# Kernel optimization log

Measured on AMD Instinct MI355X. Metric: run time of the kernel, lower is better.

The kernel has to match this reference:

```python
import jax, jax.numpy as jnp
import numpy as np

N_NODES = 4096
NUM_REL = 200
D = 32
E = 16384
B = 2048
NEG = -1e30  # finite stand-in for -inf (nan-safe under vjp)


def setup_inputs() -> dict:
    key = jax.random.key(0)
    ks = jax.random.split(key, 8)
    return {
        "edge_src": jax.random.randint(ks[0], (E,), 0, N_NODES),
        "edge_dst": jax.random.randint(ks[1], (E,), 0, N_NODES),
        "edge_type": jax.random.randint(ks[2], (E,), 0, NUM_REL),
        "neighbor_edges": jnp.arange(B),  # distinct edge ids (torch.unique output)
        "neighbor_edges2rels": jax.random.randint(ks[3], (B,), 0, NUM_REL),
        "rel_emb": jax.random.normal(ks[4], (NUM_REL, D), dtype=jnp.float32),
        "W1": jax.random.normal(ks[5], (6, D, D), dtype=jnp.float32) * 0.1,
        "b1": jax.random.normal(ks[6], (6, D), dtype=jnp.float32) * 0.1,
    }


def _masked_softmax(att):
    # att: [B, E]; entries exactly 0 are 'not connected' (torch masked_fill semantics)
    mask = att != 0
    sm = jax.nn.softmax(jnp.where(mask, att, NEG), axis=-1)
    row_has = jnp.any(mask, axis=-1, keepdims=True)
    return sm * mask * row_has  # zero masked entries and fully-empty rows (nan->0)


def reference(edge_src, edge_dst, edge_type, neighbor_edges, neighbor_edges2rels,
              rel_emb, W1, b1):
    h0 = rel_emb[edge_type]                       # [E, D] relation embedding per edge
    u = edge_src[neighbor_edges]                  # [B] head node per neighbor edge
    v = edge_dst[neighbor_edges]                  # [B] tail node per neighbor edge

    f32 = jnp.float32
    in_edge_out = (edge_dst[None, :] == u[:, None]).astype(f32)   # [B,E] in-edges of u
    out_edge_out = (edge_src[None, :] == u[:, None]).astype(f32)  # out-edges of u
    in_edge_in = (edge_dst[None, :] == v[:, None]).astype(f32)    # in-edges of v
    out_edge_in = (edge_src[None, :] == v[:, None]).astype(f32)   # out-edges of v

    edge_mode_5 = out_edge_out * in_edge_in
    edge_mode_6 = in_edge_out * out_edge_in
    out_edge_out = out_edge_out - edge_mode_5
    in_edge_in = in_edge_in - edge_mode_5
    in_edge_out = in_edge_out - edge_mode_6
    out_edge_in = out_edge_in - edge_mode_6
    modes = [in_edge_out, out_edge_out, in_edge_in, out_edge_in, edge_mode_5, edge_mode_6]

    # target-aware attention scores over all edges (aggr_flag=2, target2nei_atten)
    xxx = rel_emb[neighbor_edges2rels]            # [B, D]
    scores = jax.nn.leaky_relu(jnp.einsum('bd,ed->be', xxx, h0), negative_slope=0.2)

    agg = jnp.zeros((B, D), dtype=f32)
    for i in range(6):
        sm = _masked_softmax(modes[i] * scores)   # [B, E]
        hi = h0 @ W1[i].T + b1[i]                 # fc_reld1[i](h0), [E, D]
        agg = agg + sm @ hi
    h_0_N = jax.nn.relu(agg)                      # [B, D]

    # h1[eid] += h_0_N[i] for neighbor edges (unique ids)
    h1 = h0.at[neighbor_edges].add(h_0_N)         # [E, D]
    return h1
```

## Files before the change

### kernel.cpp

```cpp
#include <hip/hip_runtime.h>

#define D 32
#define NNODES 4096
#define CAPN 32
#define CAP 64

#define SENT_IDX (2 * NNODES + 2 * NNODES * CAPN)

__global__ void init_scatter_kernel(const int* __restrict__ edge_type,
                                    const int* __restrict__ edge_src,
                                    const int* __restrict__ edge_dst,
                                    const float* __restrict__ rel_emb,
                                    float* __restrict__ out,
                                    unsigned* __restrict__ in_cnt,
                                    unsigned* __restrict__ out_cnt,
                                    int* __restrict__ in_bkt, int* __restrict__ out_bkt,
                                    const unsigned* __restrict__ ws_base,
                                    int total4) {
    int idx = blockIdx.x * blockDim.x + threadIdx.x;
    if (idx < total4) {
        unsigned base = ws_base[SENT_IDX];
        int e = idx >> 3;
        int q = idx & 7;
        const float4* src = (const float4*)(rel_emb + edge_type[e] * D);
        ((float4*)out)[idx] = src[q];
        if (q == 0) {
            int n = edge_dst[e];
            unsigned p = atomicAdd(&in_cnt[n], 1u) - base;
            if (p < CAPN) in_bkt[n * CAPN + p] = e;
        } else if (q == 1) {
            int n = edge_src[e];
            unsigned p = atomicAdd(&out_cnt[n], 1u) - base;
            if (p < CAPN) out_bkt[n * CAPN + p] = e;
        }
    }
}

__global__ __launch_bounds__(64) void row_kernel(
        const int* __restrict__ edge_src, const int* __restrict__ edge_dst,
        const int* __restrict__ edge_type,
        const int* __restrict__ nb_edges, const int* __restrict__ nb_rels,
        const float* __restrict__ rel_emb,
        const float* __restrict__ W1, const float* __restrict__ b1,
        const unsigned* __restrict__ in_cnt, const unsigned* __restrict__ out_cnt,
        const int* __restrict__ in_bkt, const int* __restrict__ out_bkt,
        const unsigned* __restrict__ ws_base,
        float* __restrict__ out) {
    __shared__ float s_xxx[D];
    __shared__ int   s_uvne[3];
    __shared__ int   s_base[4], s_len[4], s_pref[5];
    __shared__ int   s_c[6];
    __shared__ float s_sc[6][CAP];
    __shared__ int   s_et[6][CAP];
    __shared__ float s_p[6][D];

    int tid = threadIdx.x;
    int b = blockIdx.x;

    if (tid == 0) {
        int ne = nb_edges[b];
        s_uvne[2] = ne;
        s_uvne[0] = edge_src[ne];
        s_uvne[1] = edge_dst[ne];
    }
    if (tid < D) s_xxx[tid] = rel_emb[nb_rels[b] * D + tid];
    if (tid < 6) s_c[tid] = 0;
    __syncthreads();
    const int u = s_uvne[0], v = s_uvne[1];

    if (tid < 4) {
        unsigned cbase = ws_base[SENT_IDX];
        int node = (tid < 2) ? u : v;
        bool isin = (tid & 1) == 0;
        unsigned raw = isin ? in_cnt[node] : out_cnt[node];
        unsigned len = raw - cbase;
        if (len > CAPN) len = CAPN;
        s_base[tid] = node * CAPN;
        s_len[tid] = (int)len;
    }
    __syncthreads();
    if (tid == 0) {
        int acc = 0;
        #pragma unroll
        for (int i = 0; i < 4; ++i) { s_pref[i] = acc; acc += s_len[i]; }
        s_pref[4] = acc;
    }
    __syncthreads();
    int total = s_pref[4];

    for (int idx = tid; idx < total; idx += 64) {
        int li = 0;
        while (li < 3 && idx >= s_pref[li + 1]) ++li;
        int j = idx - s_pref[li];
        int e = ((li & 1) == 0) ? in_bkt[s_base[li] + j] : out_bkt[s_base[li] + j];
        int s = edge_src[e];
        int d = edge_dst[e];
        bool own;
        if (li == 0)      own = true;
        else if (li == 1) own = (d != u);
        else if (li == 2) own = (d != u && s != u);
        else              own = (d != u && s != u && d != v);
        if (!own) continue;

        bool us = (s == u), ud = (d == u), vs = (s == v), vd = (d == v);
        unsigned mm = 0;
        if (ud && !vs) mm |= 1u;
        if (us && !vd) mm |= 2u;
        if (vd && !us) mm |= 4u;
        if (vs && !ud) mm |= 8u;
        if (us && vd)  mm |= 16u;
        if (ud && vs)  mm |= 32u;
        if (mm) {
            int et = edge_type[e];
            const float* hr = rel_emb + et * D;
            float t = 0.f;
            #pragma unroll
            for (int k = 0; k < D; ++k) t = fmaf(s_xxx[k], hr[k], t);
            float sc = (t >= 0.f) ? t : 0.2f * t;
            if (sc != 0.f) {
                #pragma unroll
                for (int i = 0; i < 6; ++i) {
                    if (mm & (1u << i)) {
                        int pos = atomicAdd(&s_c[i], 1);
                        if (pos < CAP) { s_sc[i][pos] = sc; s_et[i][pos] = et; }
                    }
                }
            }
        }
    }
    __syncthreads();

    if (tid < 6) {
        int n = s_c[tid];
        if (n > CAP) n = CAP;
        s_c[tid] = n;
        if (n > 0) {
            float m = -3.4e38f;
            for (int j = 0; j < n; ++j) m = fmaxf(m, s_sc[tid][j]);
            float z = 0.f;
            for (int j = 0; j < n; ++j) {
                float w = __expf(s_sc[tid][j] - m);
                s_sc[tid][j] = w;
                z += w;
            }
            float rz = 1.f / z;
            for (int j = 0; j < n; ++j) s_sc[tid][j] *= rz;
        }
    }
    __syncthreads();

    for (int idx = tid; idx < 6 * D; idx += 64) {
        int i = idx >> 5;
        int d = idx & 31;
        int n = s_c[i];
        float acc = 0.f;
        for (int j = 0; j < n; ++j)
            acc = fmaf(s_sc[i][j], rel_emb[s_et[i][j] * D + d], acc);
        s_p[i][d] = acc;
    }
    __syncthreads();

    if (tid < D) {
        int d = tid;
        float acc = 0.f;
        #pragma unroll
        for (int i = 0; i < 6; ++i) {
            if (s_c[i] > 0) acc += b1[i * D + d];
            const float* w = W1 + i * D * D + d * D;
            float a2 = 0.f;
            #pragma unroll
            for (int k = 0; k < D; ++k) a2 = fmaf(w[k], s_p[i][k], a2);
            acc += a2;
        }
        acc = fmaxf(acc, 0.f);
        out[s_uvne[2] * D + d] += acc;
    }
}

extern "C" void kernel_launch(void* const* d_in, const int* in_sizes, int n_in,
                              void* d_out, int out_size, void* d_ws, size_t ws_size,
                              hipStream_t stream) {
    const int*   edge_src  = (const int*)d_in[0];
    const int*   edge_dst  = (const int*)d_in[1];
    const int*   edge_type = (const int*)d_in[2];
    const int*   nb_edges  = (const int*)d_in[3];
    const int*   nb_rels   = (const int*)d_in[4];
    const float* rel_emb   = (const float*)d_in[5];
    const float* W1        = (const float*)d_in[6];
    const float* b1        = (const float*)d_in[7];
    float*       out       = (float*)d_out;

    int E = in_sizes[0];
    int B = in_sizes[3];
    int total4 = E * 8;

    unsigned* ws = (unsigned*)d_ws;
    unsigned* in_cnt  = ws;
    unsigned* out_cnt = ws + NNODES;
    int* in_bkt  = (int*)(ws + 2 * NNODES);
    int* out_bkt = in_bkt + NNODES * CAPN;

    init_scatter_kernel<<<(total4 + 255) / 256, 256, 0, stream>>>(
        edge_type, edge_src, edge_dst, rel_emb, out,
        in_cnt, out_cnt, in_bkt, out_bkt, ws, total4);
    row_kernel<<<B, 64, 0, stream>>>(
        edge_src, edge_dst, edge_type, nb_edges, nb_rels, rel_emb, W1, b1,
        in_cnt, out_cnt, in_bkt, out_bkt, ws, out);
}
```

Before: 86.54 us.

## Fuse scatter and row kernels into one cooperative kernel with grid sync

Merges the bucket-scatter kernel and the per-row attention kernel into a single cooperative launch of 256 blocks, with a grid-wide sync between the phases. Each 256-thread block packs four 64-lane warps, and each warp handles two rows. The aim is to remove the second launch and the inter-kernel gap. In exchange it adds grid-sync overhead, block-wide __syncthreads coupling between warps, and hardcoded E/B constants.

```diff
diff --git a/kernel.cpp b/kernel.cpp
--- a/kernel.cpp
+++ b/kernel.cpp
@@ -1,25 +1,35 @@
 #include <hip/hip_runtime.h>
+#include <hip/hip_cooperative_groups.h>
+
+namespace cg = cooperative_groups;
 
 #define D 32
 #define NNODES 4096
 #define CAPN 32
 #define CAP 64
+#define NBLK 256
+#define NTHR 256
+#define E_CONST 16384
+#define B_CONST 2048
 
 #define SENT_IDX (2 * NNODES + 2 * NNODES * CAPN)
 
-__global__ void init_scatter_kernel(const int* __restrict__ edge_type,
-                                    const int* __restrict__ edge_src,
-                                    const int* __restrict__ edge_dst,
-                                    const float* __restrict__ rel_emb,
-                                    float* __restrict__ out,
-                                    unsigned* __restrict__ in_cnt,
-                                    unsigned* __restrict__ out_cnt,
-                                    int* __restrict__ in_bkt, int* __restrict__ out_bkt,
-                                    const unsigned* __restrict__ ws_base,
-                                    int total4) {
-    int idx = blockIdx.x * blockDim.x + threadIdx.x;
-    if (idx < total4) {
-        unsigned base = ws_base[SENT_IDX];
+__global__ __launch_bounds__(NTHR) void fused_kernel(
+        const int* __restrict__ edge_src, const int* __restrict__ edge_dst,
+        const int* __restrict__ edge_type,
+        const int* __restrict__ nb_edges, const int* __restrict__ nb_rels,
+        const float* __restrict__ rel_emb,
+        const float* __restrict__ W1, const float* __restrict__ b1,
+        unsigned* __restrict__ in_cnt, unsigned* __restrict__ out_cnt,
+        int* __restrict__ in_bkt, int* __restrict__ out_bkt,
+        const unsigned* __restrict__ ws_base,
+        float* __restrict__ out) {
+    cg::grid_group grid = cg::this_grid();
+    const int tid = threadIdx.x;
+    const int bid = blockIdx.x;
+    const unsigned base = ws_base[SENT_IDX];
+
+    for (int idx = bid * NTHR + tid; idx < E_CONST * 8; idx += NBLK * NTHR) {
         int e = idx >> 3;
         int q = idx & 7;
         const float4* src = (const float4*)(rel_emb + edge_type[e] * D);
@@ -34,146 +44,145 @@
             if (p < CAPN) out_bkt[n * CAPN + p] = e;
         }
     }
-}
-
-__global__ __launch_bounds__(64) void row_kernel(
-        const int* __restrict__ edge_src, const int* __restrict__ edge_dst,
-        const int* __restrict__ edge_type,
-        const int* __restrict__ nb_edges, const int* __restrict__ nb_rels,
-        const float* __restrict__ rel_emb,
-        const float* __restrict__ W1, const float* __restrict__ b1,
-        const unsigned* __restrict__ in_cnt, const unsigned* __restrict__ out_cnt,
-        const int* __restrict__ in_bkt, const int* __restrict__ out_bkt,
-        const unsigned* __restrict__ ws_base,
-        float* __restrict__ out) {
-    __shared__ float s_xxx[D];
-    __shared__ int   s_uvne[3];
-    __shared__ int   s_base[4], s_len[4], s_pref[5];
-    __shared__ int   s_c[6];
-    __shared__ float s_sc[6][CAP];
-    __shared__ int   s_et[6][CAP];
-    __shared__ float s_p[6][D];
-
-    int tid = threadIdx.x;
-    int b = blockIdx.x;
-
-    if (tid == 0) {
-        int ne = nb_edges[b];
-        s_uvne[2] = ne;
-        s_uvne[0] = edge_src[ne];
-        s_uvne[1] = edge_dst[ne];
-    }
-    if (tid < D) s_xxx[tid] = rel_emb[nb_rels[b] * D + tid];
-    if (tid < 6) s_c[tid] = 0;
-    __syncthreads();
-    const int u = s_uvne[0], v = s_uvne[1];
-
-    if (tid < 4) {
-        unsigned cbase = ws_base[SENT_IDX];
-        int node = (tid < 2) ? u : v;
-        bool isin = (tid & 1) == 0;
-        unsigned raw = isin ? in_cnt[node] : out_cnt[node];
-        unsigned len = raw - cbase;
-        if (len > CAPN) len = CAPN;
-        s_base[tid] = node * CAPN;
-        s_len[tid] = (int)len;
-    }
-    __syncthreads();
-    if (tid == 0) {
-        int acc = 0;
-        #pragma unroll
-        for (int i = 0; i < 4; ++i) { s_pref[i] = acc; acc += s_len[i]; }
-        s_pref[4] = acc;
-    }
-    __syncthreads();
-    int total = s_pref[4];
-
-    for (int idx = tid; idx < total; idx += 64) {
-        int li = 0;
-        while (li < 3 && idx >= s_pref[li + 1]) ++li;
-        int j = idx - s_pref[li];
-        int e = ((li & 1) == 0) ? in_bkt[s_base[li] + j] : out_bkt[s_base[li] + j];
-        int s = edge_src[e];
-        int d = edge_dst[e];
-        bool own;
-        if (li == 0)      own = true;
-        else if (li == 1) own = (d != u);
-        else if (li == 2) own = (d != u && s != u);
-        else              own = (d != u && s != u && d != v);
-        if (!own) continue;
-
-        bool us = (s == u), ud = (d == u), vs = (s == v), vd = (d == v);
-        unsigned mm = 0;
-        if (ud && !vs) mm |= 1u;
-        if (us && !vd) mm |= 2u;
-        if (vd && !us) mm |= 4u;
-        if (vs && !ud) mm |= 8u;
-        if (us && vd)  mm |= 16u;
-        if (ud && vs)  mm |= 32u;
-        if (mm) {
-            int et = edge_type[e];
-            const float* hr = rel_emb + et * D;
-            float t = 0.f;
+
+    grid.sync();
+
+    const int wid = tid >> 6;
+    const int lane = tid & 63;
+
+    __shared__ float s_xxx[4][D];
+    __shared__ int   s_uvne[4][3];
+    __shared__ int   s_lb[4][4], s_len[4][4], s_pref[4][5];
+    __shared__ int   s_c[4][6];
+    __shared__ float s_sc[4][6][CAP];
+    __shared__ int   s_et[4][6][CAP];
+    __shared__ float s_p[4][6][D];
+
+    for (int rr = 0; rr < 2; ++rr) {
+        int b = bid * 8 + wid * 2 + rr;
+
+        if (lane == 0) {
+            int ne = nb_edges[b];
+            s_uvne[wid][2] = ne;
+            s_uvne[wid][0] = edge_src[ne];
+            s_uvne[wid][1] = edge_dst[ne];
+        }
+        if (lane < D) s_xxx[wid][lane] = rel_emb[nb_rels[b] * D + lane];
+        if (lane < 6) s_c[wid][lane] = 0;
+        __syncthreads();
+        const int u = s_uvne[wid][0], v = s_uvne[wid][1];
+
+        if (lane < 4) {
+            int node = (lane < 2) ? u : v;
+            bool isin = (lane & 1) == 0;
+            unsigned raw = isin ? in_cnt[node] : out_cnt[node];
+            unsigned len = raw - base;
+            if (len > CAPN) len = CAPN;
+            s_lb[wid][lane] = node * CAPN;
+            s_len[wid][lane] = (int)len;
+        }
+        __syncthreads();
+        if (lane == 0) {
+            int acc = 0;
             #pragma unroll
-            for (int k = 0; k < D; ++k) t = fmaf(s_xxx[k], hr[k], t);
-            float sc = (t >= 0.f) ? t : 0.2f * t;
-            if (sc != 0.f) {
+            for (int i = 0; i < 4; ++i) { s_pref[wid][i] = acc; acc += s_len[wid][i]; }
+            s_pref[wid][4] = acc;
+        }
+        __syncthreads();
+        int total = s_pref[wid][4];
+
+        for (int idx = lane; idx < total; idx += 64) {
+            int li = 0;
+            while (li < 3 && idx >= s_pref[wid][li + 1]) ++li;
+            int j = idx - s_pref[wid][li];
+            int e = ((li & 1) == 0) ? in_bkt[s_lb[wid][li] + j]
+                                    : out_bkt[s_lb[wid][li] + j];
+            int s = edge_src[e];
+            int d = edge_dst[e];
+            bool own;
+            if (li == 0)      own = true;
+            else if (li == 1) own = (d != u);
+            else if (li == 2) own = (d != u && s != u);
+            else              own = (d != u && s != u && d != v);
+            if (!own) continue;
+
+            bool us = (s == u), ud = (d == u), vs = (s == v), vd = (d == v);
+            unsigned mm = 0;
+            if (ud && !vs) mm |= 1u;
+            if (us && !vd) mm |= 2u;
+            if (vd && !us) mm |= 4u;
+            if (vs && !ud) mm |= 8u;
+            if (us && vd)  mm |= 16u;
+            if (ud && vs)  mm |= 32u;
+            if (mm) {
+                int et = edge_type[e];
+                const float* hr = rel_emb + et * D;
+                float t = 0.f;
                 #pragma unroll
-                for (int i = 0; i < 6; ++i) {
-                    if (mm & (1u << i)) {
-                        int pos = atomicAdd(&s_c[i], 1);
-                        if (pos < CAP) { s_sc[i][pos] = sc; s_et[i][pos] = et; }
+                for (int k = 0; k < D; ++k) t = fmaf(s_xxx[wid][k], hr[k], t);
+                float sc = (t >= 0.f) ? t : 0.2f * t;
+                if (sc != 0.f) {
+                    #pragma unroll
+                    for (int i = 0; i < 6; ++i) {
+                        if (mm & (1u << i)) {
+                            int pos = atomicAdd(&s_c[wid][i], 1);
+                            if (pos < CAP) {
+                                s_sc[wid][i][pos] = sc;
+                                s_et[wid][i][pos] = et;
+                            }
+                        }
                     }
                 }
             }
         }
-    }
-    __syncthreads();
-
-    if (tid < 6) {
-        int n = s_c[tid];
-        if (n > CAP) n = CAP;
-        s_c[tid] = n;
-        if (n > 0) {
-            float m = -3.4e38f;
-            for (int j = 0; j < n; ++j) m = fmaxf(m, s_sc[tid][j]);
-            float z = 0.f;
-            for (int j = 0; j < n; ++j) {
-                float w = __expf(s_sc[tid][j] - m);
-                s_sc[tid][j] = w;
-                z += w;
+        __syncthreads();
+
+        if (lane < 6) {
+            int n = s_c[wid][lane];
+            if (n > CAP) n = CAP;
+            s_c[wid][lane] = n;
+            if (n > 0) {
+                float m = -3.4e38f;
+                for (int j = 0; j < n; ++j) m = fmaxf(m, s_sc[wid][lane][j]);
+                float z = 0.f;
+                for (int j = 0; j < n; ++j) {
+                    float w = __expf(s_sc[wid][lane][j] - m);
+                    s_sc[wid][lane][j] = w;
+                    z += w;
+                }
+                float rz = 1.f / z;
+                for (int j = 0; j < n; ++j) s_sc[wid][lane][j] *= rz;
             }
-            float rz = 1.f / z;
-            for (int j = 0; j < n; ++j) s_sc[tid][j] *= rz;
-        }
-    }
-    __syncthreads();
-
-    for (int idx = tid; idx < 6 * D; idx += 64) {
-        int i = idx >> 5;
-        int d = idx & 31;
-        int n = s_c[i];
-        float acc = 0.f;
-        for (int j = 0; j < n; ++j)
-            acc = fmaf(s_sc[i][j], rel_emb[s_et[i][j] * D + d], acc);
-        s_p[i][d] = acc;
-    }
-    __syncthreads();
-
-    if (tid < D) {
-        int d = tid;
-        float acc = 0.f;
-        #pragma unroll
-        for (int i = 0; i < 6; ++i) {
-            if (s_c[i] > 0) acc += b1[i * D + d];
-            const float* w = W1 + i * D * D + d * D;
-            float a2 = 0.f;
+        }
+        __syncthreads();
+
+        for (int idx = lane; idx < 6 * D; idx += 64) {
+            int i = idx >> 5;
+            int d = idx & 31;
+            int n = s_c[wid][i];
+            float acc = 0.f;
+            for (int j = 0; j < n; ++j)
+                acc = fmaf(s_sc[wid][i][j], rel_emb[s_et[wid][i][j] * D + d], acc);
+            s_p[wid][i][d] = acc;
+        }
+        __syncthreads();
+
+        if (lane < D) {
+            int d = lane;
+            float acc = 0.f;
             #pragma unroll
-            for (int k = 0; k < D; ++k) a2 = fmaf(w[k], s_p[i][k], a2);
-            acc += a2;
-        }
-        acc = fmaxf(acc, 0.f);
-        out[s_uvne[2] * D + d] += acc;
+            for (int i = 0; i < 6; ++i) {
+                if (s_c[wid][i] > 0) acc += b1[i * D + d];
+                const float* w = W1 + i * D * D + d * D;
+                float a2 = 0.f;
+                #pragma unroll
+                for (int k = 0; k < D; ++k) a2 = fmaf(w[k], s_p[wid][i][k], a2);
+                acc += a2;
+            }
+            acc = fmaxf(acc, 0.f);
+            out[s_uvne[wid][2] * D + d] += acc;
+        }
+        __syncthreads();
     }
 }
 
@@ -190,20 +199,20 @@
     const float* b1        = (const float*)d_in[7];
     float*       out       = (float*)d_out;
 
-    int E = in_sizes[0];
-    int B = in_sizes[3];
-    int total4 = E * 8;
-
     unsigned* ws = (unsigned*)d_ws;
     unsigned* in_cnt  = ws;
     unsigned* out_cnt = ws + NNODES;
     int* in_bkt  = (int*)(ws + 2 * NNODES);
     int* out_bkt = in_bkt + NNODES * CAPN;
-
-    init_scatter_kernel<<<(total4 + 255) / 256, 256, 0, stream>>>(
-        edge_type, edge_src, edge_dst, rel_emb, out,
-        in_cnt, out_cnt, in_bkt, out_bkt, ws, total4);
-    row_kernel<<<B, 64, 0, stream>>>(
-        edge_src, edge_dst, edge_type, nb_edges, nb_rels, rel_emb, W1, b1,
-        in_cnt, out_cnt, in_bkt, out_bkt, ws, out);
+    const unsigned* ws_base = ws;
+
+    void* args[] = {
+        (void*)&edge_src, (void*)&edge_dst, (void*)&edge_type,
+        (void*)&nb_edges, (void*)&nb_rels, (void*)&rel_emb,
+        (void*)&W1, (void*)&b1,
+        (void*)&in_cnt, (void*)&out_cnt, (void*)&in_bkt, (void*)&out_bkt,
+        (void*)&ws_base, (void*)&out
+    };
+    hipLaunchCooperativeKernel((const void*)fused_kernel,
+                               dim3(NBLK), dim3(NTHR), args, 0, stream);
 }
```

After: 141.6 us. +63.6%, slower.
